# Kernel optimization log

Hardware: AMD Instinct MI355X
Metric: run time of the kernel (lower is better)

Reference implementation:

```python
import jax, jax.numpy as jnp
import numpy as np

TOP_K = 2

def setup_inputs() -> dict:
    key = jax.random.key(0)
    ks = jax.random.split(key, 5)
    B, S, D, E, R, H = 4, 2048, 1024, 8, 128, 4096
    s = 0.02
    return {
        "hidden_states": jax.random.normal(ks[0], (B, S, D), jnp.float32),
        "w_route": jax.random.normal(ks[1], (E, D, R), jnp.float32) * s,
        "w3": jax.random.normal(ks[2], (E, D, H), jnp.float32) * s,
        "wr2h": jax.random.normal(ks[3], (E, R, H), jnp.float32) * s,
        "wh2d": jax.random.normal(ks[4], (E, H, D), jnp.float32) * s,
    }

def reference(hidden_states, w_route, w3, wr2h, wh2d):
    B, S, D = hidden_states.shape
    E = w_route.shape[0]
    x = hidden_states.reshape(-1, D)                      # [N, D]
    N = x.shape[0]
    # per-expert routing activations (also reused as w1_state inside experts)
    acts = jnp.einsum('nd,edr->ner', x, w_route)          # [N, E, R]
    norms = jnp.linalg.norm(acts, axis=-1)                # [N, E] router logits
    probs = jax.nn.softmax(norms.astype(jnp.float32), axis=-1)
    topw, sel = jax.lax.top_k(probs, TOP_K)               # [N, k]
    topw = topw / topw.sum(axis=-1, keepdims=True)
    topw = topw.astype(x.dtype)
    # dense combine weights: routing weight if expert selected, else 0
    combine = jnp.zeros((N, E), x.dtype).at[jnp.arange(N)[:, None], sel].add(topw)
    out = jnp.zeros_like(x)
    for e in range(E):  # fixed small expert count
        h = (x @ w3[e]) * jax.nn.silu(acts[:, e, :] @ wr2h[e])  # [N, H]
        out = out + (h @ wh2d[e]) * combine[:, e:e + 1]
    final = out.reshape(B, S, D)
    # load balancing loss on the router logits (expert_act_norms)
    mask = jax.nn.one_hot(sel, E, dtype=jnp.float32)      # [N, k, E]
    tokens_per_expert = mask.mean(axis=0)                 # [k, E]
    router_prob_per_expert = probs.mean(axis=0)           # [E]
    bl_loss = jnp.sum(tokens_per_expert * router_prob_per_expert[None, :]) * E
    return final, norms, bl_loss
```

## Files before the change

kernel.cpp:

```cpp
#include <hip/hip_runtime.h>


#define DEV static __device__ __forceinline__

typedef float  f32x4  __attribute__((ext_vector_type(4)));
typedef __bf16 bf16x8 __attribute__((ext_vector_type(8)));

#define VMCNT_(n) asm volatile("s_waitcnt vmcnt(" #n ")" ::: "memory")
#define VMCNT(n) VMCNT_(n)
#define SBAR()   asm volatile("s_barrier" ::: "memory")

DEV unsigned short f2bf(float f) {
  union { float f; unsigned u; } v; v.f = f;
  unsigned r = v.u + 0x7fffu + ((v.u >> 16) & 1u);
  return (unsigned short)(r >> 16);
}
DEV float bf2f(unsigned short b) {
  union { unsigned u; float f; } v; v.u = ((unsigned)b) << 16;
  return v.f;
}

DEV void gll16(const void* g, void* l) {
  __builtin_amdgcn_global_load_lds(
      (const __attribute__((address_space(1))) unsigned int*)g,
      (__attribute__((address_space(3))) unsigned int*)l, 16, 0, 0);
}

DEV f32x4 mfma16(bf16x8 a, bf16x8 b, f32x4 c) {
  return __builtin_amdgcn_mfma_f32_16x16x32_bf16(a, b, c, 0, 0, 0);
}

DEV int xcd_swz_gen(int bid, int nwg) {
  int x = bid & 7, o = bid >> 3;
  int q = nwg >> 3, r = nwg & 7;
  return (x < r ? x * (q + 1) : r * (q + 1) + (x - r) * q) + o;
}

DEV int swz_slot(int s) {
  int p = s >> 3, w0 = (s & 7) ^ (p & 7);
  return (((p << 1) | (w0 >> 2)) << 2) | (w0 & 3);
}
DEV bf16x8 frag_read32(const unsigned short* lds, int row, int lg) {
  int p = row >> 1;
  int off = p * 128 + (((((row & 1) << 2) | lg) ^ (p & 7)) << 4);
  return *(const bf16x8*)((const char*)lds + off);
}

DEV bf16x8 frag_read(const unsigned short* lds, int row, int kb) {
  int off = row * 128 + ((kb * 2) ^ ((row & 7) << 4));
  return *(const bf16x8*)((const char*)lds + off);
}
DEV void stage_linear(const unsigned short* base, size_t pitch, int k0,
                      unsigned short* lds, int tid) {
  int wq = tid >> 6, lane = tid & 63;
#pragma unroll
  for (int i = 0; i < 4; ++i) {
    int s = wq * 256 + i * 64 + lane;
    int row = s >> 3, b = s & 7;
    int bb = b ^ (row & 7);
    const unsigned short* g = base + (size_t)row * pitch + (size_t)(k0 + bb * 8);
    gll16(g, lds + (size_t)(wq * 256 + i * 64) * 8);
  }
}
DEV void mfma_block(const unsigned short* A, const unsigned short* B,
                    f32x4 (&acc)[4][4], int wm, int wn, int lg, int lc) {
#pragma unroll
  for (int ks = 0; ks < 2; ++ks) {
    int kb = ks * 32 + lg * 8;
    bf16x8 af[4], bff[4];
#pragma unroll
    for (int i = 0; i < 4; ++i) {
      af[i]  = frag_read(A, wm * 64 + i * 16 + lc, kb);
      bff[i] = frag_read(B, wn * 64 + i * 16 + lc, kb);
    }
#pragma unroll
    for (int mf = 0; mf < 4; ++mf)
#pragma unroll
      for (int nf = 0; nf < 4; ++nf)
        acc[mf][nf] = mfma16(af[mf], bff[nf], acc[mf][nf]);
  }
}


__global__ __launch_bounds__(256) void k_cast_x(const float* __restrict__ x,
    unsigned short* __restrict__ xh, unsigned short* __restrict__ xl) {
  int stride = gridDim.x * blockDim.x;
  for (int i = blockIdx.x * blockDim.x + threadIdx.x; i < 8192 * 1024 / 4;
       i += stride) {
    float4 v = ((const float4*)x)[i];
    ushort4 h, l;
    h.x = f2bf(v.x); l.x = f2bf(v.x - bf2f(h.x));
    h.y = f2bf(v.y); l.y = f2bf(v.y - bf2f(h.y));
    h.z = f2bf(v.z); l.z = f2bf(v.z - bf2f(h.z));
    h.w = f2bf(v.w); l.w = f2bf(v.w - bf2f(h.w));
    ((ushort4*)xh)[i] = h;
    ((ushort4*)xl)[i] = l;
  }
}

__global__ void k_zero(int* cnt, float* probsum) {
  int t = threadIdx.x;
  if (t < 16) cnt[t] = 0;
  if (t < 8)  probsum[t] = 0.f;
}

__global__ __launch_bounds__(256) void k_transp(const float* __restrict__ src,
    unsigned short* __restrict__ dst, int K, int N) {
  int ntn = N >> 6;
  int kt = blockIdx.x / ntn, nt = blockIdx.x % ntn;
  int e = blockIdx.y;
  __shared__ float tl[64][65];
  const float* s = src + (size_t)e * K * N;
  unsigned short* d = dst + (size_t)e * N * K;
  int tid = threadIdx.x;
  int c4 = (tid & 15) * 4, rr = tid >> 4;
#pragma unroll
  for (int p = 0; p < 4; ++p) {
    int row = rr + p * 16;
    float4 v = *(const float4*)(s + (size_t)(kt * 64 + row) * N + nt * 64 + c4);
    tl[row][c4] = v.x; tl[row][c4 + 1] = v.y;
    tl[row][c4 + 2] = v.z; tl[row][c4 + 3] = v.w;
  }
  __syncthreads();
#pragma unroll
  for (int p = 0; p < 4; ++p) {
    int n = rr + p * 16;
    ushort4 o;
    o.x = f2bf(tl[c4 + 0][n]); o.y = f2bf(tl[c4 + 1][n]);
    o.z = f2bf(tl[c4 + 2][n]); o.w = f2bf(tl[c4 + 3][n]);
    *(ushort4*)(d + (size_t)(nt * 64 + n) * K + kt * 64 + c4) = o;
  }
}

__global__ __launch_bounds__(256) void k_transp_split(const float* __restrict__ src,
    unsigned short* __restrict__ dh, unsigned short* __restrict__ dl, int K, int N) {
  int ntn = N >> 6;
  int kt = blockIdx.x / ntn, nt = blockIdx.x % ntn;
  int e = blockIdx.y;
  __shared__ float tl[64][65];
  const float* s = src + (size_t)e * K * N;
  size_t dbase = (size_t)e * N * K;
  int tid = threadIdx.x;
  int c4 = (tid & 15) * 4, rr = tid >> 4;
#pragma unroll
  for (int p = 0; p < 4; ++p) {
    int row = rr + p * 16;
    float4 v = *(const float4*)(s + (size_t)(kt * 64 + row) * N + nt * 64 + c4);
    tl[row][c4] = v.x; tl[row][c4 + 1] = v.y;
    tl[row][c4 + 2] = v.z; tl[row][c4 + 3] = v.w;
  }
  __syncthreads();
#pragma unroll
  for (int p = 0; p < 4; ++p) {
    int n = rr + p * 16;
    ushort4 oh, ol;
#pragma unroll
    for (int i = 0; i < 4; ++i) {
      float v = tl[c4 + i][n];
      unsigned short hh = f2bf(v);
      unsigned short ll = f2bf(v - bf2f(hh));
      ((unsigned short*)&oh)[i] = hh;
      ((unsigned short*)&ol)[i] = ll;
    }
    *(ushort4*)(dh + dbase + (size_t)(nt * 64 + n) * K + kt * 64 + c4) = oh;
    *(ushort4*)(dl + dbase + (size_t)(nt * 64 + n) * K + kt * 64 + c4) = ol;
  }
}

__global__ __launch_bounds__(256) void k_route_gemm(
    const unsigned short* __restrict__ xh, const unsigned short* __restrict__ xl,
    const unsigned short* __restrict__ wrh_t, const unsigned short* __restrict__ wrl_t,
    unsigned short* __restrict__ acts, float* __restrict__ norms_out) {
  __shared__ __align__(16) unsigned short Ah[128 * 64], Al[128 * 64];
  __shared__ __align__(16) unsigned short Bh[128 * 64], Bl[128 * 64];
  __shared__ float ssq_s[128][2];
  int tid = threadIdx.x;
  int mt = blockIdx.x, e = blockIdx.y;
  int wq = tid >> 6, lane = tid & 63;
  int wm = wq >> 1, wn = wq & 1, lg = lane >> 4, lc = lane & 15;
  f32x4 acc[4][4] = {};
  const unsigned short* ah_src = xh + (size_t)mt * 128 * 1024;
  const unsigned short* al_src = xl + (size_t)mt * 128 * 1024;
  const unsigned short* bh_src = wrh_t + (size_t)e * 128 * 1024;
  const unsigned short* bl_src = wrl_t + (size_t)e * 128 * 1024;
  for (int kt = 0; kt < 16; ++kt) {
    int k0 = kt * 64;
    stage_linear(ah_src, 1024, k0, Ah, tid);
    stage_linear(al_src, 1024, k0, Al, tid);
    stage_linear(bh_src, 1024, k0, Bh, tid);
    stage_linear(bl_src, 1024, k0, Bl, tid);
    __syncthreads();
#pragma unroll
    for (int ks = 0; ks < 2; ++ks) {
      int kb = ks * 32 + lg * 8;
      bf16x8 ahf[4], alf[4], bhf[4], blf[4];
#pragma unroll
      for (int i = 0; i < 4; ++i) {
        ahf[i] = frag_read(Ah, wm * 64 + i * 16 + lc, kb);
        alf[i] = frag_read(Al, wm * 64 + i * 16 + lc, kb);
        bhf[i] = frag_read(Bh, wn * 64 + i * 16 + lc, kb);
        blf[i] = frag_read(Bl, wn * 64 + i * 16 + lc, kb);
      }
#pragma unroll
      for (int mf = 0; mf < 4; ++mf)
#pragma unroll
        for (int nf = 0; nf < 4; ++nf) {
          acc[mf][nf] = mfma16(ahf[mf], bhf[nf], acc[mf][nf]);
          acc[mf][nf] = mfma16(alf[mf], bhf[nf], acc[mf][nf]);
          acc[mf][nf] = mfma16(ahf[mf], blf[nf], acc[mf][nf]);
        }
    }
    __syncthreads();
  }
  float ssq[4][4];
#pragma unroll
  for (int mf = 0; mf < 4; ++mf)
#pragma unroll
    for (int r = 0; r < 4; ++r) ssq[mf][r] = 0.f;
#pragma unroll
  for (int mf = 0; mf < 4; ++mf)
#pragma unroll
    for (int nf = 0; nf < 4; ++nf)
#pragma unroll
      for (int r = 0; r < 4; ++r) {
        float v = acc[mf][nf][r];
        int row = wm * 64 + mf * 16 + lg * 4 + r;
        int col = wn * 64 + nf * 16 + lc;
        acts[(size_t)(mt * 128 + row) * 1024 + e * 128 + col] = f2bf(v);
        ssq[mf][r] += v * v;
      }
#pragma unroll
  for (int mf = 0; mf < 4; ++mf)
#pragma unroll
    for (int r = 0; r < 4; ++r) {
      float s = ssq[mf][r];
      s += __shfl_xor(s, 1); s += __shfl_xor(s, 2);
      s += __shfl_xor(s, 4); s += __shfl_xor(s, 8);
      if (lc == 0) ssq_s[wm * 64 + mf * 16 + lg * 4 + r][wn] = s;
    }
  __syncthreads();
  if (tid < 128) {
    float s = ssq_s[tid][0] + ssq_s[tid][1];
    norms_out[(size_t)(mt * 128 + tid) * 8 + e] = sqrtf(s);
  }
}

__global__ __launch_bounds__(256) void k_router(const float* __restrict__ norms,
    float* __restrict__ topw, int* __restrict__ sel,
    int* __restrict__ cnt, float* __restrict__ probsum) {
  __shared__ float ps_s[8];
  __shared__ int cnt_s[16];
  int tid = threadIdx.x;
  if (tid < 8)  ps_s[tid] = 0.f;
  if (tid < 16) cnt_s[tid] = 0;
  __syncthreads();
  int n = blockIdx.x * 256 + tid;
  float p[8], mx = -3.4e38f;
#pragma unroll
  for (int e = 0; e < 8; ++e) { p[e] = norms[(size_t)n * 8 + e]; mx = fmaxf(mx, p[e]); }
  float s = 0.f;
#pragma unroll
  for (int e = 0; e < 8; ++e) { p[e] = __expf(p[e] - mx); s += p[e]; }
  float inv = 1.f / s;
  int i1 = 0; float v1 = p[0];
#pragma unroll
  for (int e = 1; e < 8; ++e) if (p[e] > v1) { v1 = p[e]; i1 = e; }
  int i2 = -1; float v2 = -1.f;
#pragma unroll
  for (int e = 0; e < 8; ++e) if (e != i1 && p[e] > v2) { v2 = p[e]; i2 = e; }
  float wsum = v1 + v2;
  topw[n * 2 + 0] = v1 / wsum;
  topw[n * 2 + 1] = v2 / wsum;
  sel[n * 2 + 0] = i1;
  sel[n * 2 + 1] = i2;
  atomicAdd(&cnt_s[i1], 1);
  atomicAdd(&cnt_s[8 + i2], 1);
#pragma unroll
  for (int e = 0; e < 8; ++e) atomicAdd(&ps_s[e], p[e] * inv);
  __syncthreads();
  if (tid < 8)  atomicAdd(&probsum[tid], ps_s[tid]);
  if (tid < 16) atomicAdd(&cnt[tid], cnt_s[tid]);
}

__global__ void k_plan(const int* __restrict__ cnt, const float* __restrict__ probsum,
                       int* __restrict__ offs, int* __restrict__ fill,
                       int4* __restrict__ tilemap, float* __restrict__ bl_out) {
  int4* map256 = tilemap;
  int4* map128 = tilemap + 80;
  int t = 0;
  for (int k = 0; k < 2; ++k) {
    int pos = 0;
    for (int e = 0; e < 8; ++e) {
      int c = cnt[k * 8 + e];
      offs[k * 8 + e] = pos;
      int ntl = (c + 255) >> 8;
      for (int i = 0; i < ntl; ++i) {
        int rr = c - i * 256; if (rr > 256) rr = 256;
        map256[t] = make_int4(e, k * 8192 + pos + i * 256, rr, 0);
        ++t;
      }
      pos += c;
    }
  }
  for (; t < 80; ++t) map256[t] = make_int4(0, 0, 0, 0);
  for (int i = 0; i < 80; ++i) {
    int4 m = map256[i];
    for (int h = 0; h < 2; ++h) {
      int r = m.z - h * 128;
      if (r < 0) r = 0; if (r > 128) r = 128;
      map128[i * 2 + h] = make_int4(m.x, m.y + h * 128, r, i * 256 + h * 128);
    }
  }
  for (int i = 0; i < 16; ++i) fill[i] = 0;
  float bl = 0.f;
  for (int e = 0; e < 8; ++e)
    bl += ((float)(cnt[e] + cnt[8 + e]) / 8192.f) * (probsum[e] / 8192.f);
  *bl_out = bl * 8.f;
}

__global__ __launch_bounds__(256) void k_fill(const int* __restrict__ sel,
    const float* __restrict__ topw, const int* __restrict__ offs,
    int* __restrict__ fill, int* __restrict__ list01, float* __restrict__ wlist) {
  int n = blockIdx.x * 256 + threadIdx.x;
#pragma unroll
  for (int k = 0; k < 2; ++k) {
    int e = sel[n * 2 + k];
    int pos = atomicAdd(&fill[k * 8 + e], 1);
    int idx = k * 8192 + offs[k * 8 + e] + pos;
    list01[idx] = n;
    wlist[idx] = topw[n * 2 + k];
  }
}

__global__ __launch_bounds__(512, 2) void k_gemm1(
    const unsigned short* __restrict__ xh, const unsigned short* __restrict__ acts,
    const unsigned short* __restrict__ w3t, const unsigned short* __restrict__ wr2h_t,
    const int* __restrict__ list, const int4* __restrict__ tilemap, int tile_lo,
    int nt, unsigned short* __restrict__ hbuf) {
  __shared__ __align__(16) unsigned short SA[3][256 * 32];
  __shared__ __align__(16) unsigned short SB[3][128 * 32];
  __shared__ int toks[256];
  int wg = xcd_swz_gen((int)blockIdx.x, nt * 32);
  int tloc = wg >> 5, bn = wg & 31;
  int4 ent = tilemap[tile_lo + tloc];
  int e = ent.x, posbase = ent.y, rows = ent.z;
  if (rows == 0) return;
  int tid = threadIdx.x;
  if (tid < 256) {
    int rr = tid < rows ? tid : rows - 1;
    toks[tid] = list[posbase + rr];
  }
  __syncthreads();
  int wq = tid >> 6, lane = tid & 63;
  int wm = wq >> 1, wn = wq & 1, lg = lane >> 4, lc = lane & 15;
  int sA0 = wq * 128 + lane, sA1 = sA0 + 64;
  int sB0 = wq * 64 + lane;
  int vA0 = swz_slot(sA0), vA1 = swz_slot(sA1), vB0 = swz_slot(sB0);
  const unsigned short* gA0 = xh + (size_t)toks[vA0 >> 2] * 1024 + (vA0 & 3) * 8;
  const unsigned short* gA1 = xh + (size_t)toks[vA1 >> 2] * 1024 + (vA1 & 3) * 8;
  const unsigned short* qA0 = acts + (size_t)toks[vA0 >> 2] * 1024 + e * 128 + (vA0 & 3) * 8;
  const unsigned short* qA1 = acts + (size_t)toks[vA1 >> 2] * 1024 + e * 128 + (vA1 & 3) * 8;
  const unsigned short* gB0 =
      w3t + ((size_t)e * 4096 + bn * 128 + (vB0 >> 2)) * 1024 + (vB0 & 3) * 8;
  const unsigned short* qB0 =
      wr2h_t + ((size_t)e * 4096 + bn * 128 + (vB0 >> 2)) * 128 + (vB0 & 3) * 8;
  f32x4 acc_a[4][4] = {}, acc_s[4][4] = {};

  auto stage1 = [&](int tt, int bs) {
    unsigned short* dA0 = &SA[bs][(size_t)sA0 * 8];
    unsigned short* dA1 = &SA[bs][(size_t)sA1 * 8];
    unsigned short* dB0 = &SB[bs][(size_t)sB0 * 8];
    if (tt < 32) {
      int k0 = tt * 32;
      gll16(gA0 + k0, dA0); gll16(gA1 + k0, dA1); gll16(gB0 + k0, dB0);
    } else {
      int k0 = (tt - 32) * 32;
      gll16(qA0 + k0, dA0); gll16(qA1 + k0, dA1); gll16(qB0 + k0, dB0);
    }
  };

  stage1(0, 0); stage1(1, 1);
  int cur = 0, bs = 2;

#define G1_TILE(VMN, DO_STAGE, STT, ACC)                                     \
  {                                                                          \
    VMCNT(VMN); SBAR();                                                      \
    bf16x8 af[4], bf[4];                                                     \
    _Pragma("unroll") for (int i = 0; i < 4; ++i)                            \
      af[i] = frag_read32(&SA[cur][0], wm * 64 + i * 16 + lc, lg);           \
    _Pragma("unroll") for (int i = 0; i < 4; ++i)                            \
      bf[i] = frag_read32(&SB[cur][0], wn * 64 + i * 16 + lc, lg);           \
    if (DO_STAGE) stage1(STT, bs);                                           \
    SBAR();                                                                  \
    __builtin_amdgcn_s_setprio(1);                                           \
    _Pragma("unroll") for (int mf = 0; mf < 4; ++mf)                         \
      _Pragma("unroll") for (int nf = 0; nf < 4; ++nf)                       \
        ACC[mf][nf] = mfma16(af[mf], bf[nf], ACC[mf][nf]);                   \
    __builtin_amdgcn_s_setprio(0);                                           \
    cur = cur == 2 ? 0 : cur + 1;                                            \
    bs  = bs  == 2 ? 0 : bs  + 1;                                            \
  }

  for (int t = 0; t < 32; ++t) G1_TILE(3, true, t + 2, acc_a);
  G1_TILE(3, true, 34, acc_s);
  G1_TILE(3, true, 35, acc_s);
  G1_TILE(3, false, 0, acc_s);
  G1_TILE(0, false, 0, acc_s);
#undef G1_TILE

  size_t hrow0 = (size_t)tloc * 256;
#pragma unroll
  for (int mf = 0; mf < 4; ++mf)
#pragma unroll
    for (int nf = 0; nf < 4; ++nf)
#pragma unroll
      for (int r = 0; r < 4; ++r) {
        int row = wm * 64 + mf * 16 + lg * 4 + r;
        if (row < rows) {
          int col = wn * 64 + nf * 16 + lc;
          float sv = acc_s[mf][nf][r];
          float hv = acc_a[mf][nf][r] * (sv / (1.f + __expf(-sv)));
          hbuf[(hrow0 + row) * 4096 + (size_t)bn * 128 + col] = f2bf(hv);
        }
      }
}

__global__ __launch_bounds__(512, 2) void k_gemm2(
    const unsigned short* __restrict__ hbuf, const unsigned short* __restrict__ wh2dt,
    const int* __restrict__ list, const float* __restrict__ wlist,
    const int4* __restrict__ map128, int tile_lo, int nt,
    float* __restrict__ out) {
  __shared__ __align__(16) unsigned short SA[3][128 * 32];
  __shared__ __align__(16) unsigned short SB[3][256 * 32];
  __shared__ int toks[128];
  __shared__ float wr_s[128];
  int wg = xcd_swz_gen((int)blockIdx.x, nt * 8);
  int tloc = wg >> 2, bn = wg & 3;
  int4 ent = map128[tile_lo * 2 + tloc];
  int e = ent.x, posbase = ent.y, rows = ent.z;
  if (rows == 0) return;
  int hb = ent.w - tile_lo * 256;
  int tid = threadIdx.x;
  if (tid < 128) {
    int rr = tid < rows ? tid : rows - 1;
    toks[tid] = list[posbase + rr];
    wr_s[tid] = wlist[posbase + rr];
  }
  __syncthreads();
  int wq = tid >> 6, lane = tid & 63;
  int wm = wq >> 2, wn = wq & 3, lg = lane >> 4, lc = lane & 15;
  int sA0 = wq * 64 + lane;
  int sB0 = wq * 128 + lane, sB1 = sB0 + 64;
  int vA0 = swz_slot(sA0), vB0 = swz_slot(sB0), vB1 = swz_slot(sB1);
  const unsigned short* gA0 = hbuf + (size_t)(hb + (vA0 >> 2)) * 4096 + (vA0 & 3) * 8;
  const unsigned short* gB0 =
      wh2dt + ((size_t)e * 1024 + bn * 256 + (vB0 >> 2)) * 4096 + (vB0 & 3) * 8;
  const unsigned short* gB1 =
      wh2dt + ((size_t)e * 1024 + bn * 256 + (vB1 >> 2)) * 4096 + (vB1 & 3) * 8;
  f32x4 acc[4][4] = {};

  auto stage2 = [&](int tt, int bs) {
    int k0 = tt * 32;
    gll16(gA0 + k0, &SA[bs][(size_t)sA0 * 8]);
    gll16(gB0 + k0, &SB[bs][(size_t)sB0 * 8]);
    gll16(gB1 + k0, &SB[bs][(size_t)sB1 * 8]);
  };

  stage2(0, 0); stage2(1, 1);
  int cur = 0, bs = 2;

#define G2_TILE(VMN, DO_STAGE, STT)                                          \
  {                                                                          \
    VMCNT(VMN); SBAR();                                                      \
    bf16x8 af[4], bf[4];                                                     \
    _Pragma("unroll") for (int i = 0; i < 4; ++i)                            \
      af[i] = frag_read32(&SA[cur][0], wm * 64 + i * 16 + lc, lg);           \
    _Pragma("unroll") for (int i = 0; i < 4; ++i)                            \
      bf[i] = frag_read32(&SB[cur][0], wn * 64 + i * 16 + lc, lg);           \
    if (DO_STAGE) stage2(STT, bs);                                           \
    SBAR();                                                                  \
    __builtin_amdgcn_s_setprio(1);                                           \
    _Pragma("unroll") for (int mf = 0; mf < 4; ++mf)                         \
      _Pragma("unroll") for (int nf = 0; nf < 4; ++nf)                       \
        acc[mf][nf] = mfma16(af[mf], bf[nf], acc[mf][nf]);                   \
    __builtin_amdgcn_s_setprio(0);                                           \
    cur = cur == 2 ? 0 : cur + 1;                                            \
    bs  = bs  == 2 ? 0 : bs  + 1;                                            \
  }

  for (int t = 0; t < 126; ++t) G2_TILE(3, true, t + 2);
  G2_TILE(3, false, 0);
  G2_TILE(0, false, 0);
#undef G2_TILE

#pragma unroll
  for (int mf = 0; mf < 4; ++mf)
#pragma unroll
    for (int nf = 0; nf < 4; ++nf)
#pragma unroll
      for (int r = 0; r < 4; ++r) {
        int row = wm * 64 + mf * 16 + lg * 4 + r;
        if (row < rows) {
          int col = wn * 64 + nf * 16 + lc;
          float v = acc[mf][nf][r] * wr_s[row];
          atomicAdd(out + (size_t)toks[row] * 1024 + bn * 256 + col, v);
        }
      }
}


extern "C" void kernel_launch(void* const* d_in, const int* in_sizes, int n_in,
                              void* d_out, int out_size, void* d_ws, size_t ws_size,
                              hipStream_t stream) {
  (void)in_sizes; (void)n_in; (void)out_size;
  const float* x      = (const float*)d_in[0];
  const float* wroute = (const float*)d_in[1];
  const float* w3     = (const float*)d_in[2];
  const float* wr2h   = (const float*)d_in[3];
  const float* wh2d   = (const float*)d_in[4];
  float* out = (float*)d_out;

  char* ws = (char*)d_ws;
  size_t off = 0;
  auto carve = [&](size_t bytes) -> void* {
    void* p = ws + off; off += (bytes + 255) & ~(size_t)255; return p;
  };
  unsigned short* xh     = (unsigned short*)carve((size_t)8192 * 1024 * 2);
  unsigned short* xl     = (unsigned short*)carve((size_t)8192 * 1024 * 2);
  unsigned short* wrh_t  = (unsigned short*)carve((size_t)8 * 128 * 1024 * 2);
  unsigned short* wrl_t  = (unsigned short*)carve((size_t)8 * 128 * 1024 * 2);
  unsigned short* w3t    = (unsigned short*)carve((size_t)8 * 4096 * 1024 * 2);
  unsigned short* wr2h_t = (unsigned short*)carve((size_t)8 * 4096 * 128 * 2);
  unsigned short* wh2dt  = (unsigned short*)carve((size_t)8 * 1024 * 4096 * 2);
  unsigned short* acts   = (unsigned short*)carve((size_t)8192 * 1024 * 2);
  int*   list01 = (int*)carve(2 * 8192 * 4);
  float* wlist  = (float*)carve(2 * 8192 * 4);
  int*   sel    = (int*)carve(8192 * 2 * 4);
  float* topw   = (float*)carve(8192 * 2 * 4);
  int*   ctr    = (int*)carve(8192);
  int* cnt = ctr; int* fill = ctr + 16; int* offs = ctr + 32;
  float* probsum = (float*)(ctr + 48);
  int4* tilemap = (int4*)(ctr + 64);

  size_t avail = ws_size > off ? ws_size - off : 0;
  int tpc = 0;
  const int cands[4] = {80, 40, 20, 10};
  for (int i = 0; i < 4; ++i) {
    if ((size_t)cands[i] * 256 * 4096 * 2 <= avail) { tpc = cands[i]; break; }
  }
  if (!tpc) return;
  unsigned short* hbuf = (unsigned short*)(ws + off);

  float* norms_out = out + 8388608;
  float* bl_out    = out + 8454144;

  hipMemsetAsync(out, 0, (size_t)8388608 * 4, stream);
  k_cast_x<<<2048, 256, 0, stream>>>(x, xh, xl);
  k_zero<<<1, 64, 0, stream>>>(cnt, probsum);
  k_transp<<<dim3(16 * 64, 8), 256, 0, stream>>>(w3, w3t, 1024, 4096);
  k_transp<<<dim3(64 * 16, 8), 256, 0, stream>>>(wh2d, wh2dt, 4096, 1024);
  k_transp<<<dim3(2 * 64, 8), 256, 0, stream>>>(wr2h, wr2h_t, 128, 4096);
  k_transp_split<<<dim3(16 * 2, 8), 256, 0, stream>>>(wroute, wrh_t, wrl_t, 1024, 128);
  k_route_gemm<<<dim3(64, 8), 256, 0, stream>>>(xh, xl, wrh_t, wrl_t, acts, norms_out);
  k_router<<<32, 256, 0, stream>>>(norms_out, topw, sel, cnt, probsum);
  k_plan<<<1, 1, 0, stream>>>(cnt, probsum, offs, fill, tilemap, bl_out);
  k_fill<<<32, 256, 0, stream>>>(sel, topw, offs, fill, list01, wlist);

  int nchunk = (80 + tpc - 1) / tpc;
  for (int c = 0; c < nchunk; ++c) {
    int tile_lo = c * tpc;
    int nt = 80 - tile_lo < tpc ? 80 - tile_lo : tpc;
    k_gemm1<<<nt * 32, 512, 0, stream>>>(
        xh, acts, w3t, wr2h_t, list01, tilemap, tile_lo, nt, hbuf);
    k_gemm2<<<nt * 8, 512, 0, stream>>>(
        hbuf, wh2dt, list01, wlist, tilemap + 80, tile_lo, nt, out);
  }
}
```

Measured before the change: 859.1 us.

## Switch expert GEMMs from triple to double buffering with one barrier per step

Replaces the three-stage LDS pipeline with two-stage double buffering in both expert GEMM kernels. Each step now issues the next tile's global-to-LDS load, computes on the current buffer, then waits for all loads and barriers once. The LDS slot assignment becomes linear in thread id, gemm2's launch bounds ask for four blocks per CU, and an unused helper is removed. Using less LDS and fewer barriers is meant to raise occupancy and cut sync overhead, at the cost of a shallower prefetch that may expose more memory latency.

```diff
diff --git a/kernel.cpp b/kernel.cpp
--- a/kernel.cpp
+++ b/kernel.cpp
@@ -6,9 +6,8 @@
 typedef float  f32x4  __attribute__((ext_vector_type(4)));
 typedef __bf16 bf16x8 __attribute__((ext_vector_type(8)));
 
-#define VMCNT_(n) asm volatile("s_waitcnt vmcnt(" #n ")" ::: "memory")
-#define VMCNT(n) VMCNT_(n)
-#define SBAR()   asm volatile("s_barrier" ::: "memory")
+#define VMCNT0() asm volatile("s_waitcnt vmcnt(0)" ::: "memory")
+#define SBAR()   __builtin_amdgcn_s_barrier()
 
 DEV unsigned short f2bf(float f) {
   union { float f; unsigned u; } v; v.f = f;
@@ -60,24 +59,6 @@
     int bb = b ^ (row & 7);
     const unsigned short* g = base + (size_t)row * pitch + (size_t)(k0 + bb * 8);
     gll16(g, lds + (size_t)(wq * 256 + i * 64) * 8);
-  }
-}
-DEV void mfma_block(const unsigned short* A, const unsigned short* B,
-                    f32x4 (&acc)[4][4], int wm, int wn, int lg, int lc) {
-#pragma unroll
-  for (int ks = 0; ks < 2; ++ks) {
-    int kb = ks * 32 + lg * 8;
-    bf16x8 af[4], bff[4];
-#pragma unroll
-    for (int i = 0; i < 4; ++i) {
-      af[i]  = frag_read(A, wm * 64 + i * 16 + lc, kb);
-      bff[i] = frag_read(B, wn * 64 + i * 16 + lc, kb);
-    }
-#pragma unroll
-    for (int mf = 0; mf < 4; ++mf)
-#pragma unroll
-      for (int nf = 0; nf < 4; ++nf)
-        acc[mf][nf] = mfma16(af[mf], bff[nf], acc[mf][nf]);
   }
 }
 
@@ -337,8 +318,8 @@
     const unsigned short* __restrict__ w3t, const unsigned short* __restrict__ wr2h_t,
     const int* __restrict__ list, const int4* __restrict__ tilemap, int tile_lo,
     int nt, unsigned short* __restrict__ hbuf) {
-  __shared__ __align__(16) unsigned short SA[3][256 * 32];
-  __shared__ __align__(16) unsigned short SB[3][128 * 32];
+  __shared__ __align__(16) unsigned short SA[2][256 * 32];
+  __shared__ __align__(16) unsigned short SB[2][128 * 32];
   __shared__ int toks[256];
   int wg = xcd_swz_gen((int)blockIdx.x, nt * 32);
   int tloc = wg >> 5, bn = wg & 31;
@@ -353,8 +334,8 @@
   __syncthreads();
   int wq = tid >> 6, lane = tid & 63;
   int wm = wq >> 1, wn = wq & 1, lg = lane >> 4, lc = lane & 15;
-  int sA0 = wq * 128 + lane, sA1 = sA0 + 64;
-  int sB0 = wq * 64 + lane;
+  int sA0 = tid, sA1 = tid + 512;
+  int sB0 = tid;
   int vA0 = swz_slot(sA0), vA1 = swz_slot(sA1), vB0 = swz_slot(sB0);
   const unsigned short* gA0 = xh + (size_t)toks[vA0 >> 2] * 1024 + (vA0 & 3) * 8;
   const unsigned short* gA1 = xh + (size_t)toks[vA1 >> 2] * 1024 + (vA1 & 3) * 8;
@@ -379,34 +360,32 @@
     }
   };
 
-  stage1(0, 0); stage1(1, 1);
-  int cur = 0, bs = 2;
-
-#define G1_TILE(VMN, DO_STAGE, STT, ACC)                                     \
+  stage1(0, 0);
+  VMCNT0();
+  SBAR();
+  int cur = 0;
+
+#define G1_STEP(T, ACC, DOSTAGE)                                             \
   {                                                                          \
-    VMCNT(VMN); SBAR();                                                      \
-    bf16x8 af[4], bf[4];                                                     \
+    if (DOSTAGE) stage1((T) + 1, cur ^ 1);                                   \
+    bf16x8 af[4], bv[4];                                                     \
     _Pragma("unroll") for (int i = 0; i < 4; ++i)                            \
       af[i] = frag_read32(&SA[cur][0], wm * 64 + i * 16 + lc, lg);           \
     _Pragma("unroll") for (int i = 0; i < 4; ++i)                            \
-      bf[i] = frag_read32(&SB[cur][0], wn * 64 + i * 16 + lc, lg);           \
-    if (DO_STAGE) stage1(STT, bs);                                           \
-    SBAR();                                                                  \
+      bv[i] = frag_read32(&SB[cur][0], wn * 64 + i * 16 + lc, lg);           \
     __builtin_amdgcn_s_setprio(1);                                           \
     _Pragma("unroll") for (int mf = 0; mf < 4; ++mf)                         \
       _Pragma("unroll") for (int nf = 0; nf < 4; ++nf)                       \
-        ACC[mf][nf] = mfma16(af[mf], bf[nf], ACC[mf][nf]);                   \
+        ACC[mf][nf] = mfma16(af[mf], bv[nf], ACC[mf][nf]);                   \
     __builtin_amdgcn_s_setprio(0);                                           \
-    cur = cur == 2 ? 0 : cur + 1;                                            \
-    bs  = bs  == 2 ? 0 : bs  + 1;                                            \
-  }
-
-  for (int t = 0; t < 32; ++t) G1_TILE(3, true, t + 2, acc_a);
-  G1_TILE(3, true, 34, acc_s);
-  G1_TILE(3, true, 35, acc_s);
-  G1_TILE(3, false, 0, acc_s);
-  G1_TILE(0, false, 0, acc_s);
-#undef G1_TILE
+    VMCNT0();                                                                \
+    SBAR();                                                                  \
+    cur ^= 1;                                                                \
+  }
+
+  for (int t = 0; t < 32; ++t) G1_STEP(t, acc_a, true);
+  for (int t = 32; t < 36; ++t) G1_STEP(t, acc_s, t < 35);
+#undef G1_STEP
 
   size_t hrow0 = (size_t)tloc * 256;
 #pragma unroll
@@ -425,13 +404,13 @@
       }
 }
 
-__global__ __launch_bounds__(512, 2) void k_gemm2(
+__global__ __launch_bounds__(512, 4) void k_gemm2(
     const unsigned short* __restrict__ hbuf, const unsigned short* __restrict__ wh2dt,
     const int* __restrict__ list, const float* __restrict__ wlist,
     const int4* __restrict__ map128, int tile_lo, int nt,
     float* __restrict__ out) {
-  __shared__ __align__(16) unsigned short SA[3][128 * 32];
-  __shared__ __align__(16) unsigned short SB[3][256 * 32];
+  __shared__ __align__(16) unsigned short SA[2][128 * 32];
+  __shared__ __align__(16) unsigned short SB[2][256 * 32];
   __shared__ int toks[128];
   __shared__ float wr_s[128];
   int wg = xcd_swz_gen((int)blockIdx.x, nt * 8);
@@ -449,8 +428,8 @@
   __syncthreads();
   int wq = tid >> 6, lane = tid & 63;
   int wm = wq >> 2, wn = wq & 3, lg = lane >> 4, lc = lane & 15;
-  int sA0 = wq * 64 + lane;
-  int sB0 = wq * 128 + lane, sB1 = sB0 + 64;
+  int sA0 = tid;
+  int sB0 = tid, sB1 = tid + 512;
   int vA0 = swz_slot(sA0), vB0 = swz_slot(sB0), vB1 = swz_slot(sB1);
   const unsigned short* gA0 = hbuf + (size_t)(hb + (vA0 >> 2)) * 4096 + (vA0 & 3) * 8;
   const unsigned short* gB0 =
@@ -466,32 +445,31 @@
     gll16(gB1 + k0, &SB[bs][(size_t)sB1 * 8]);
   };
 
-  stage2(0, 0); stage2(1, 1);
-  int cur = 0, bs = 2;
-
-#define G2_TILE(VMN, DO_STAGE, STT)                                          \
-  {                                                                          \
-    VMCNT(VMN); SBAR();                                                      \
-    bf16x8 af[4], bf[4];                                                     \
-    _Pragma("unroll") for (int i = 0; i < 4; ++i)                            \
-      af[i] = frag_read32(&SA[cur][0], wm * 64 + i * 16 + lc, lg);           \
-    _Pragma("unroll") for (int i = 0; i < 4; ++i)                            \
-      bf[i] = frag_read32(&SB[cur][0], wn * 64 + i * 16 + lc, lg);           \
-    if (DO_STAGE) stage2(STT, bs);                                           \
-    SBAR();                                                                  \
-    __builtin_amdgcn_s_setprio(1);                                           \
-    _Pragma("unroll") for (int mf = 0; mf < 4; ++mf)                         \
-      _Pragma("unroll") for (int nf = 0; nf < 4; ++nf)                       \
-        acc[mf][nf] = mfma16(af[mf], bf[nf], acc[mf][nf]);                   \
-    __builtin_amdgcn_s_setprio(0);                                           \
-    cur = cur == 2 ? 0 : cur + 1;                                            \
-    bs  = bs  == 2 ? 0 : bs  + 1;                                            \
-  }
-
-  for (int t = 0; t < 126; ++t) G2_TILE(3, true, t + 2);
-  G2_TILE(3, false, 0);
-  G2_TILE(0, false, 0);
-#undef G2_TILE
+  stage2(0, 0);
+  VMCNT0();
+  SBAR();
+  int cur = 0;
+
+  for (int t = 0; t < 128; ++t) {
+    if (t < 127) stage2(t + 1, cur ^ 1);
+    bf16x8 af[4], bv[4];
+#pragma unroll
+    for (int i = 0; i < 4; ++i)
+      af[i] = frag_read32(&SA[cur][0], wm * 64 + i * 16 + lc, lg);
+#pragma unroll
+    for (int i = 0; i < 4; ++i)
+      bv[i] = frag_read32(&SB[cur][0], wn * 64 + i * 16 + lc, lg);
+    __builtin_amdgcn_s_setprio(1);
+#pragma unroll
+    for (int mf = 0; mf < 4; ++mf)
+#pragma unroll
+      for (int nf = 0; nf < 4; ++nf)
+        acc[mf][nf] = mfma16(af[mf], bv[nf], acc[mf][nf]);
+    __builtin_amdgcn_s_setprio(0);
+    VMCNT0();
+    SBAR();
+    cur ^= 1;
+  }
 
 #pragma unroll
   for (int mf = 0; mf < 4; ++mf)
```

New measurement: 902.2 us. +5.0%, slower.
